# Kernel optimization log

Measured on AMD Instinct MI355X. Metric: run time of the kernel, lower is better.

The kernel has to match this reference:

```python
import jax, jax.numpy as jnp
import numpy as np
from jax import lax


def _ln(x, g, b, eps=1e-5):
    m = jnp.mean(x, axis=-1, keepdims=True)
    v = jnp.mean((x - m) ** 2, axis=-1, keepdims=True)
    return (x - m) / jnp.sqrt(v + eps) * g + b


def _lin(x, w, b):  # torch Linear: w [out,in]
    return x @ w.T + b


def _conv(x, w, b, stride, pad):
    y = lax.conv_general_dilated(x, w, (stride, stride), pad,
                                 dimension_numbers=('NCHW', 'OIHW', 'NCHW'))
    return y + b[None, :, None, None]


def _haar_dwt(x):
    # J=1 haar, zero mode, even H/W: per 2x2 block [[a,b],[c,d]]
    a = x[:, :, 0::2, 0::2]
    bb = x[:, :, 0::2, 1::2]
    c = x[:, :, 1::2, 0::2]
    d = x[:, :, 1::2, 1::2]
    ll = (a + bb + c + d) * 0.5
    lohi = (a - bb + c - d) * 0.5  # band 0 (col-high)
    hilo = (a + bb - c - d) * 0.5  # band 1 (row-high)
    hihi = (a - bb - c + d) * 0.5  # band 2
    return ll, lohi, hilo, hihi


def _cross_attention(q, k, v):
    # q,k,v: [b, d, c]; 8 equal chunks along d; softmax over QUERY axis (torch dim=1)
    b, d, c = q.shape
    chunk = d // 8
    qc = q.reshape(b, 8, chunk, c)
    kc = k.reshape(b, 8, chunk, c)
    vc = v.reshape(b, 8, chunk, c)
    att = jnp.einsum('bnqc,bnkc->bnqk', qc, kc) * (8.0 ** -0.5)
    att = jax.nn.softmax(att, axis=2)  # normalize over q (matches F.softmax dim=1)
    out = jnp.einsum('bnqk,bnkc->bnqc', att, vc)
    return out.reshape(b, d, c)


def _ffn(x, ln1_g, ln1_b, fc1_w, fc1_b, div_w, div_b, fc2_w, fc2_b,
         ln3_g, ln3_b, fc3a_w, fc3a_b, fc3b_w, fc3b_b, lnn_g, lnn_b, act_w, act_b):
    x1 = jax.nn.gelu(_lin(_ln(x, ln1_g, ln1_b), fc1_w, fc1_b), approximate=False)
    x2 = jax.nn.gelu(_lin(x, div_w, div_b), approximate=False) - x1
    x2 = jax.nn.gelu(_lin(x2, fc2_w, fc2_b), approximate=False)
    x3 = _lin(jax.nn.gelu(_lin(_ln(x, ln3_g, ln3_b), fc3a_w, fc3a_b), approximate=False), fc3b_w, fc3b_b)
    gate = jax.nn.sigmoid(_lin(x, act_w, act_b))
    # dropout(0.5) is identity in eval mode
    return gate * _ln(x2 + x3, lnn_g, lnn_b)


def _resize_bilinear_ac(x, oh, ow):
    # bilinear, align_corners=True
    B, C, H, W = x.shape
    def idx(n_in, n_out):
        pos = jnp.linspace(0.0, n_in - 1.0, n_out)
        i0 = jnp.floor(pos).astype(jnp.int32)
        i1 = jnp.minimum(i0 + 1, n_in - 1)
        return i0, i1, (pos - i0).astype(x.dtype)
    y0, y1, wy = idx(H, oh)
    x0, x1, wx = idx(W, ow)
    r = x[:, :, y0, :] * (1 - wy)[None, None, :, None] + x[:, :, y1, :] * wy[None, None, :, None]
    return r[:, :, :, x0] * (1 - wx)[None, None, None, :] + r[:, :, :, x1] * wx[None, None, None, :]


def setup_inputs() -> dict:
    key = jax.random.key(0)
    ks = jax.random.split(key, 25)
    B, Cin, H, W = 16, 128, 128, 128
    Ch = 128  # out_planes // 2
    def nrm(k, shp, s=0.02):
        return jax.random.normal(k, shp, jnp.float32) * s
    inp = {
        'x': jax.random.normal(ks[0], (B, Cin, H, W), jnp.float32),
        'conv1_w': nrm(ks[1], (Ch, 2 * Cin, 1, 1)), 'conv1_b': jnp.zeros((Ch,), jnp.float32),
        'l1_w': nrm(ks[2], (Ch, Cin, 4, 4)), 'l1_b': jnp.zeros((Ch,), jnp.float32),
        'ln1_g': jnp.ones((Ch,), jnp.float32), 'ln1_b': jnp.zeros((Ch,), jnp.float32),
        'fc1_w': nrm(ks[3], (Ch, Ch)), 'fc1_b': jnp.zeros((Ch,), jnp.float32),
        'div_w': nrm(ks[4], (Ch, Ch)), 'div_b': jnp.zeros((Ch,), jnp.float32),
        'fc2_w': nrm(ks[5], (Ch, Ch)), 'fc2_b': jnp.zeros((Ch,), jnp.float32),
        'ln3_g': jnp.ones((Ch,), jnp.float32), 'ln3_b': jnp.zeros((Ch,), jnp.float32),
        'fc3a_w': nrm(ks[6], (Ch, Ch)), 'fc3a_b': jnp.zeros((Ch,), jnp.float32),
        'fc3b_w': nrm(ks[7], (Ch, Ch)), 'fc3b_b': jnp.zeros((Ch,), jnp.float32),
        'lnn_g': jnp.ones((Ch,), jnp.float32), 'lnn_b': jnp.zeros((Ch,), jnp.float32),
        'act_w': nrm(ks[8], (Ch, Ch)), 'act_b': jnp.zeros((Ch,), jnp.float32),
    }
    return inp


def reference(x, conv1_w, conv1_b, l1_w, l1_b, ln1_g, ln1_b, fc1_w, fc1_b,
              div_w, div_b, fc2_w, fc2_b, ln3_g, ln3_b, fc3a_w, fc3a_b,
              fc3b_w, fc3b_b, lnn_g, lnn_b, act_w, act_b):
    dw = jax.nn.relu(_conv(x, l1_w, l1_b, 2, ((1, 1), (1, 1))))
    yL, y_HL, y_LH, y_HH = _haar_dwt(x)
    y = _conv(jnp.concatenate((y_HL, y_LH), axis=1), conv1_w, conv1_b, 1, ((0, 0), (0, 0)))
    b, c, h, w = y.shape
    y_t = y.transpose(0, 2, 3, 1).reshape(b, h * w, c)
    yL_t = yL.transpose(0, 2, 3, 1).reshape(b, h * w, c)
    yHH_t = y_HH.transpose(0, 2, 3, 1).reshape(b, h * w, c)
    att = _cross_attention(yL_t, y_t, yHH_t)
    att = _ffn(att, ln1_g, ln1_b, fc1_w, fc1_b, div_w, div_b, fc2_w, fc2_b,
               ln3_g, ln3_b, fc3a_w, fc3a_b, fc3b_w, fc3b_b, lnn_g, lnn_b, act_w, act_b)
    att = att.reshape(b, h, w, c).transpose(0, 3, 1, 2)
    y_img = y_t.reshape(b, h, w, c).transpose(0, 3, 1, 2)
    down_2x = _resize_bilinear_ac(x, h, w)
    att = att * (down_2x - dw)
    return att + y_img
```

## Files before the change

### kernel.cpp

```cpp
#include <hip/hip_runtime.h>
#include <cmath>


#define EPI_NONE 0
#define EPI_GELU 1
#define EPI_GELU_SUB 2
#define EPI_ADD 3
#define EPI_SIGMOID 4
#define EPI_EXP 5

typedef unsigned short u16;
typedef __bf16 v8bf __attribute__((ext_vector_type(8)));
typedef float f32x4 __attribute__((ext_vector_type(4)));

__device__ __forceinline__ float gelu_f(float v) {
  return 0.5f * v * (1.f + erff(v * 0.70710678118654752f));
}
__device__ __forceinline__ float sigmoid_f(float v) {
  return 1.f / (1.f + __expf(-v));
}
__device__ __forceinline__ float bf2f(u16 h) {
  return __uint_as_float((unsigned)h << 16);
}
__device__ __forceinline__ u16 f2bf(float f) {
  unsigned u = __float_as_uint(f);
  return (u16)((u + 0x7fffu + ((u >> 16) & 1u)) >> 16);
}
__device__ __forceinline__ unsigned f2bf_pk(float lo, float hi) {
  unsigned a = __float_as_uint(lo), b = __float_as_uint(hi);
  a = (a + 0x7fffu + ((a >> 16) & 1u)) >> 16;
  b = (b + 0x7fffu + ((b >> 16) & 1u)) >> 16;
  return a | (b << 16);
}

__global__ __launch_bounds__(256) void pre_k(const float* __restrict__ x,
                                             u16* __restrict__ yL16,
                                             u16* __restrict__ yHHt16,
                                             u16* __restrict__ hllh16) {
  int gx = blockIdx.x;
  int jt = gx & 1, cit = gx >> 1;
  int i = blockIdx.y, b = blockIdx.z;
  int j0 = jt * 32, ci0 = cit * 32;
  int tx = threadIdx.x & 31, ty = threadIdx.x >> 5;
  __shared__ float sll[32][33], shl[32][33], slh[32][33], shh[32][33];
  const float2* x2 = (const float2*)x;
#pragma unroll
  for (int k = 0; k < 4; ++k) {
    int ci = ty + 8 * k;
    long base = (((long)b * 128 + ci0 + ci) * 128 + 2 * i) * 64 + j0 + tx;
    float2 ab = x2[base];
    float2 cd = x2[base + 64];
    float a = ab.x, bb = ab.y, c = cd.x, d = cd.y;
    sll[ci][tx] = (a + bb + c + d) * 0.5f;
    shl[ci][tx] = (a - bb + c - d) * 0.5f;
    slh[ci][tx] = (a + bb - c - d) * 0.5f;
    shh[ci][tx] = (a - bb - c + d) * 0.5f;
  }
  __syncthreads();
  long tok = (long)b * 4096 + i * 64 + j0;
#pragma unroll
  for (int k = 0; k < 4; ++k) {
    int row = ty + 8 * k;
    long t = tok + row;
    yL16[t * 128 + ci0 + tx] = f2bf(sll[tx][row]);
    hllh16[t * 256 + ci0 + tx] = f2bf(shl[tx][row]);
    hllh16[t * 256 + 128 + ci0 + tx] = f2bf(slh[tx][row]);
    yHHt16[(long)(ci0 + row) * 65536 + tok + tx] = f2bf(shh[row][tx]);
  }
}

__global__ __launch_bounds__(256) void wcvt8_k(
    const float* __restrict__ a0, const float* __restrict__ a1,
    const float* __restrict__ a2, const float* __restrict__ a3,
    const float* __restrict__ a4, const float* __restrict__ a5,
    const float* __restrict__ a6, const float* __restrict__ a7,
    unsigned* __restrict__ dst) {
  int f = blockIdx.x * 256 + threadIdx.x;
  int e = 2 * f;
  const float* s; int b;
  if (e < 262144)      { s = a0; b = 0; }
  else if (e < 294912) { s = a1; b = 262144; }
  else if (e < 311296) { s = a2; b = 294912; }
  else if (e < 327680) { s = a3; b = 311296; }
  else if (e < 344064) { s = a4; b = 327680; }
  else if (e < 360448) { s = a5; b = 344064; }
  else if (e < 376832) { s = a6; b = 360448; }
  else                 { s = a7; b = 376832; }
  dst[f] = f2bf_pk(s[e - b], s[e - b + 1]);
}

template <int AMODE, int EPI>
__global__ __launch_bounds__(256) void gemm16_k(
    const u16* __restrict__ A, long sA, int lda,
    const u16* __restrict__ B, long sB, int ldb,
    u16* __restrict__ C, long sC, int ldc,
    int K, float alpha, const float* __restrict__ bias,
    const u16* __restrict__ aux, const float* __restrict__ sc) {
  __shared__ __align__(16) char smem[32768];
  char* As = smem;
  char* Bs = smem + 16384;
  int z = blockIdx.z;
  int tid = threadIdx.x, lane = tid & 63, w = tid >> 6;
  int wm = w >> 1, wn = w & 1, l15 = lane & 15, l4 = lane >> 4;
  const u16* Ab = A + (long)z * sA + (long)blockIdx.x * 128 * lda;
  const u16* Bb = B + (long)z * sB + (long)blockIdx.y * 128 * ldb;
  const float* scz = (AMODE == 1) ? sc + (long)z * K : nullptr;
  int sm = tid >> 3, skg = tid & 7;
  int sbase = sm * 128 + ((skg ^ (sm & 7)) << 4);
  uint4 pa[4], pb[4];

  auto loadAB = [&](int k0) {
#pragma unroll
    for (int u = 0; u < 4; ++u) {
      pb[u] = *(const uint4*)(Bb + (long)(sm + 32 * u) * ldb + k0 + skg * 8);
      uint4 v = *(const uint4*)(Ab + (long)(sm + 32 * u) * lda + k0 + skg * 8);
      if (AMODE == 1) {
        float4 s0 = *(const float4*)(scz + k0 + skg * 8);
        float4 s1 = *(const float4*)(scz + k0 + skg * 8 + 4);
        v.x = f2bf_pk(bf2f((u16)(v.x & 0xffff)) * s0.x, bf2f((u16)(v.x >> 16)) * s0.y);
        v.y = f2bf_pk(bf2f((u16)(v.y & 0xffff)) * s0.z, bf2f((u16)(v.y >> 16)) * s0.w);
        v.z = f2bf_pk(bf2f((u16)(v.z & 0xffff)) * s1.x, bf2f((u16)(v.z >> 16)) * s1.y);
        v.w = f2bf_pk(bf2f((u16)(v.w & 0xffff)) * s1.z, bf2f((u16)(v.w >> 16)) * s1.w);
      }
      pa[u] = v;
    }
  };

  f32x4 acc[4][4] = {};
  loadAB(0);
  int nch = K >> 6;
  for (int ch = 0; ch < nch; ++ch) {
    __syncthreads();
#pragma unroll
    for (int u = 0; u < 4; ++u) {
      *(uint4*)(As + sbase + u * 4096) = pa[u];
      *(uint4*)(Bs + sbase + u * 4096) = pb[u];
    }
    __syncthreads();
    if (ch + 1 < nch) loadAB((ch + 1) << 6);
#pragma unroll
    for (int s = 0; s < 2; ++s) {
      int ko = (((s << 2) | l4) ^ (l15 & 7)) << 4;
      v8bf af[4], bfr[4];
#pragma unroll
      for (int t = 0; t < 4; ++t) {
        af[t] = *(const v8bf*)(As + (64 * wm + 16 * t + l15) * 128 + ko);
        bfr[t] = *(const v8bf*)(Bs + (64 * wn + 16 * t + l15) * 128 + ko);
      }
#pragma unroll
      for (int mt = 0; mt < 4; ++mt)
#pragma unroll
        for (int nt = 0; nt < 4; ++nt)
          acc[mt][nt] = __builtin_amdgcn_mfma_f32_16x16x32_bf16(af[mt], bfr[nt], acc[mt][nt], 0, 0, 0);
    }
  }
  u16* Cb = C + (long)z * sC;
#pragma unroll
  for (int mt = 0; mt < 4; ++mt) {
#pragma unroll
    for (int nt = 0; nt < 4; ++nt) {
      f32x4 a = acc[mt][nt];
      int n = blockIdx.y * 128 + 64 * wn + 16 * nt + l15;
      float bv = bias ? bias[n] : 0.f;
#pragma unroll
      for (int r = 0; r < 4; ++r) {
        long m = (long)blockIdx.x * 128 + 64 * wm + 16 * mt + 4 * l4 + r;
        float v = a[r] * alpha + bv;
        if (EPI == EPI_GELU) v = gelu_f(v);
        else if (EPI == EPI_GELU_SUB) v = gelu_f(v) - bf2f(aux[m * ldc + n]);
        else if (EPI == EPI_ADD) v += bf2f(aux[m * ldc + n]);
        else if (EPI == EPI_SIGMOID) v = sigmoid_f(v);
        else if (EPI == EPI_EXP) v = __expf(v);
        Cb[m * ldc + n] = f2bf(v);
      }
    }
  }
}

__global__ __launch_bounds__(256) void conv4m_k(const float* __restrict__ x,
                                                const u16* __restrict__ wb,
                                                const float* __restrict__ bias,
                                                u16* __restrict__ dw16) {
  __shared__ __align__(16) char smem[36864];
  char* As = smem;
  char* Ws = smem + 18432;
  int ib = blockIdx.x, b = blockIdx.y;
  int tid = threadIdx.x;
  int lane = tid & 63, w = tid >> 6;
  int wm = w >> 1, wn = w & 1;
  int l15 = lane & 15, l4 = lane >> 4;
  f32x4 acc[4][4] = {};
  const float* xb = x + (long)b * 128 * 128 * 128;

  int m = tid & 127, qp0 = tid >> 7;
  int col0 = 2 * (m & 63) - 1;
  int oi_a = 2 * ib + (m >> 6);
  int groff = 2 * oi_a - 1;
  bool c0ok = (m & 63) != 0;
  bool c3ok = (m & 63) != 63;
  int awo[8];
#pragma unroll
  for (int it = 0; it < 8; ++it) awo[it] = m * 144 + (qp0 + 2 * it) * 8;
  const u16* wgbase = wb + (long)(tid >> 1) * 2048 + (tid & 1) * 32;
  int wro = (tid >> 1) * 144 + (tid & 1) * 64;

  uint4 wreg[4];
  uint2 areg[8];
  auto preW = [&](int ch) {
    const uint4* src = (const uint4*)(wgbase + ch * 64);
#pragma unroll
    for (int u = 0; u < 4; ++u) wreg[u] = src[u];
  };
  auto preA = [&](int ch) {
#pragma unroll
    for (int it = 0; it < 8; ++it) {
      int qp = qp0 + 2 * it;
      int c = qp >> 2, kh = qp & 3;
      int gr = groff + kh;
      const float* row = xb + ((long)(4 * ch + c) * 128 + gr) * 128;
      bool rok = (unsigned)gr < 128u;
      float v0 = (rok && c0ok) ? row[col0] : 0.f;
      float v1 = rok ? row[col0 + 1] : 0.f;
      float v2 = rok ? row[col0 + 2] : 0.f;
      float v3 = (rok && c3ok) ? row[col0 + 3] : 0.f;
      areg[it].x = f2bf_pk(v0, v1);
      areg[it].y = f2bf_pk(v2, v3);
    }
  };

  preW(0);
  preA(0);
  for (int ch = 0; ch < 32; ++ch) {
    __syncthreads();
    {
      uint4* dst = (uint4*)(Ws + wro);
#pragma unroll
      for (int u = 0; u < 4; ++u) dst[u] = wreg[u];
#pragma unroll
      for (int it = 0; it < 8; ++it) *(uint2*)(As + awo[it]) = areg[it];
    }
    __syncthreads();
    if (ch < 31) { preW(ch + 1); preA(ch + 1); }
#pragma unroll
    for (int s = 0; s < 2; ++s) {
      v8bf af[4], bfr[4];
#pragma unroll
      for (int t = 0; t < 4; ++t) {
        af[t] = *(const v8bf*)(As + (64 * wm + 16 * t + l15) * 144 + s * 64 + l4 * 16);
        bfr[t] = *(const v8bf*)(Ws + (64 * wn + 16 * t + l15) * 144 + s * 64 + l4 * 16);
      }
#pragma unroll
      for (int mt = 0; mt < 4; ++mt)
#pragma unroll
        for (int nt = 0; nt < 4; ++nt)
          acc[mt][nt] = __builtin_amdgcn_mfma_f32_16x16x32_bf16(af[mt], bfr[nt], acc[mt][nt], 0, 0, 0);
    }
  }
  __syncthreads();
  float* buf = (float*)(smem + w * 4352);
  int oi = 2 * ib + wm;
#pragma unroll
  for (int cg = 0; cg < 4; ++cg) {
    int co = 64 * wn + 16 * cg + l15;
    float bv = bias[co];
#pragma unroll
    for (int mt = 0; mt < 4; ++mt) {
      f32x4 a = acc[mt][cg];
#pragma unroll
      for (int r = 0; r < 4; ++r)
        buf[l15 * 65 + 16 * mt + 4 * l4 + r] = fmaxf(a[r] + bv, 0.f);
    }
    __syncthreads();
#pragma unroll
    for (int cr = 0; cr < 16; ++cr) {
      dw16[(((long)b * 128 + 64 * wn + 16 * cg + cr) * 64 + oi) * 64 + lane] =
          f2bf(buf[cr * 65 + lane]);
    }
    __syncthreads();
  }
}

__global__ __launch_bounds__(256) void ssum_k(const u16* __restrict__ E,
                                              float* __restrict__ sc) {
  int z = blockIdx.y;
  int k = blockIdx.x * 256 + threadIdx.x;
  const u16* Eb = E + (long)z * 262144 + k;
  float s = 0.f;
#pragma unroll 8
  for (int q = 0; q < 512; ++q) s += bf2f(Eb[(long)q * 512]);
  sc[(long)z * 512 + k] = 1.f / s;
}

__global__ __launch_bounds__(256) void ln16_k(const u16* __restrict__ X,
                                              const float* __restrict__ g,
                                              const float* __restrict__ bt,
                                              const u16* __restrict__ gate,
                                              u16* __restrict__ Y) {
  int t = (blockIdx.x * 256 + threadIdx.x) >> 6;
  int lane = threadIdx.x & 63;
  const u16* xr = X + (long)t * 128;
  float v0 = bf2f(xr[lane]), v1 = bf2f(xr[lane + 64]);
  float s = v0 + v1, sq = v0 * v0 + v1 * v1;
#pragma unroll
  for (int off = 32; off > 0; off >>= 1) {
    s += __shfl_xor(s, off);
    sq += __shfl_xor(sq, off);
  }
  float mean = s * 0.0078125f;
  float var = sq * 0.0078125f - mean * mean;
  float rstd = rsqrtf(var + 1e-5f);
  float y0 = (v0 - mean) * rstd * g[lane] + bt[lane];
  float y1 = (v1 - mean) * rstd * g[lane + 64] + bt[lane + 64];
  if (gate) {
    y0 *= bf2f(gate[(long)t * 128 + lane]);
    y1 *= bf2f(gate[(long)t * 128 + lane + 64]);
  }
  Y[(long)t * 128 + lane] = f2bf(y0);
  Y[(long)t * 128 + lane + 64] = f2bf(y1);
}

__global__ __launch_bounds__(256) void combine_k(const u16* __restrict__ attf,
                                                 const u16* __restrict__ yt,
                                                 const u16* __restrict__ dw16,
                                                 const float* __restrict__ x,
                                                 float* __restrict__ out) {
  int gx = blockIdx.x;
  int jt = gx & 1, cot = gx >> 1;
  int i = blockIdx.y, b = blockIdx.z;
  int j0 = jt * 32, co0 = cot * 32;
  int tx = threadIdx.x & 31, ty = threadIdx.x >> 5;
  __shared__ float sa[32][33], sy[32][33];
  long tokbase = (long)b * 4096 + i * 64 + j0;
#pragma unroll
  for (int k = 0; k < 4; ++k) {
    int row = ty + 8 * k;
    long idx = (tokbase + row) * 128 + co0 + tx;
    sa[row][tx] = bf2f(attf[idx]);
    sy[row][tx] = bf2f(yt[idx]);
  }
  __syncthreads();
  float py = (float)(i * 127) / 63.0f;
  int y0 = (int)py;
  int y1 = min(y0 + 1, 127);
  float wy = py - (float)y0;
  int j = j0 + tx;
  float px = (float)(j * 127) / 63.0f;
  int x0 = (int)px;
  int x1 = min(x0 + 1, 127);
  float wx = px - (float)x0;
#pragma unroll
  for (int k = 0; k < 4; ++k) {
    int co = co0 + ty + 8 * k;
    const float* xb = x + (((long)b * 128 + co) * 128) * 128;
    float r0 = xb[y0 * 128 + x0] * (1.f - wx) + xb[y0 * 128 + x1] * wx;
    float r1 = xb[y1 * 128 + x0] * (1.f - wx) + xb[y1 * 128 + x1] * wx;
    float d2 = r0 * (1.f - wy) + r1 * wy;
    long oidx = (((long)b * 128 + co) * 64 + i) * 64 + j;
    float dwv = bf2f(dw16[oidx]);
    out[oidx] = sa[tx][ty + 8 * k] * (d2 - dwv) + sy[tx][ty + 8 * k];
  }
}

extern "C" void kernel_launch(void* const* d_in, const int* in_sizes, int n_in,
                              void* d_out, int out_size, void* d_ws, size_t ws_size,
                              hipStream_t stream) {
  const float* x = (const float*)d_in[0];
  const float* w1 = (const float*)d_in[1];
  const float* b1 = (const float*)d_in[2];
  const float* l1w = (const float*)d_in[3];
  const float* l1b = (const float*)d_in[4];
  const float* ln1g = (const float*)d_in[5];
  const float* ln1b = (const float*)d_in[6];
  const float* fc1w = (const float*)d_in[7];
  const float* fc1b = (const float*)d_in[8];
  const float* divw = (const float*)d_in[9];
  const float* divb = (const float*)d_in[10];
  const float* fc2w = (const float*)d_in[11];
  const float* fc2b = (const float*)d_in[12];
  const float* ln3g = (const float*)d_in[13];
  const float* ln3b = (const float*)d_in[14];
  const float* fc3aw = (const float*)d_in[15];
  const float* fc3ab = (const float*)d_in[16];
  const float* fc3bw = (const float*)d_in[17];
  const float* fc3bb = (const float*)d_in[18];
  const float* lnng = (const float*)d_in[19];
  const float* lnnb = (const float*)d_in[20];
  const float* actw = (const float*)d_in[21];
  const float* actb = (const float*)d_in[22];

  char* W = (char*)d_ws;
  u16* yL16 = (u16*)(W);
  u16* hllh16 = (u16*)(W + 16777216L);
  u16* yHHt16 = (u16*)(W + 50331648L);
  u16* y16 = (u16*)(W + 67108864L);
  u16* S16 = (u16*)(W + 83886080L);
  u16* attO16 = (u16*)(W + 150994944L);
  u16* dw16 = (u16*)(W + 167772160L);
  u16* t1 = (u16*)(W + 184549376L);
  u16* t2 = (u16*)(W + 201326592L);
  u16* t3 = (u16*)(W + 218103808L);
  u16* t4 = (u16*)(W + 234881024L);
  float* sc = (float*)(W + 251658240L);
  u16* wall = (u16*)(W + 251920384L);
  u16* l1wb = wall;
  u16* w1b = wall + 262144;
  u16* fc1b16 = wall + 294912;
  u16* divb16 = wall + 311296;
  u16* fc2b16 = wall + 327680;
  u16* fc3ab16 = wall + 344064;
  u16* fc3bb16 = wall + 360448;
  u16* actb16 = wall + 376832;

  dim3 blk(256);
  const float qk_scale = 0.35355339059327373f;

  wcvt8_k<<<dim3(768), blk, 0, stream>>>(l1w, w1, fc1w, divw, fc2w, fc3aw,
                                         fc3bw, actw, (unsigned*)wall);
  pre_k<<<dim3(8, 64, 16), blk, 0, stream>>>(x, yL16, yHHt16, hllh16);
  gemm16_k<0, EPI_NONE><<<dim3(512, 1, 1), blk, 0, stream>>>(
      hllh16, 0, 256, w1b, 0, 256, y16, 0, 128, 256, 1.f, b1, nullptr, nullptr);
  conv4m_k<<<dim3(32, 16), blk, 0, stream>>>(x, l1wb, l1b, dw16);
  gemm16_k<0, EPI_EXP><<<dim3(4, 4, 128), blk, 0, stream>>>(
      yL16, 65536, 128, y16, 65536, 128, S16, 262144, 512, 128, qk_scale,
      nullptr, nullptr, nullptr);
  ssum_k<<<dim3(2, 128), blk, 0, stream>>>(S16, sc);
  gemm16_k<1, EPI_NONE><<<dim3(4, 1, 128), blk, 0, stream>>>(
      S16, 262144, 512, yHHt16, 512, 65536, attO16, 65536, 128, 512, 1.f,
      nullptr, nullptr, sc);
  ln16_k<<<16384, blk, 0, stream>>>(attO16, ln1g, ln1b, nullptr, t1);
  gemm16_k<0, EPI_GELU><<<dim3(512, 1, 1), blk, 0, stream>>>(
      t1, 0, 128, fc1b16, 0, 128, t2, 0, 128, 128, 1.f, fc1b, nullptr, nullptr);
  gemm16_k<0, EPI_GELU_SUB><<<dim3(512, 1, 1), blk, 0, stream>>>(
      attO16, 0, 128, divb16, 0, 128, t3, 0, 128, 128, 1.f, divb, t2, nullptr);
  gemm16_k<0, EPI_GELU><<<dim3(512, 1, 1), blk, 0, stream>>>(
      t3, 0, 128, fc2b16, 0, 128, t4, 0, 128, 128, 1.f, fc2b, nullptr, nullptr);
  ln16_k<<<16384, blk, 0, stream>>>(attO16, ln3g, ln3b, nullptr, t1);
  gemm16_k<0, EPI_GELU><<<dim3(512, 1, 1), blk, 0, stream>>>(
      t1, 0, 128, fc3ab16, 0, 128, t3, 0, 128, 128, 1.f, fc3ab, nullptr, nullptr);
  gemm16_k<0, EPI_ADD><<<dim3(512, 1, 1), blk, 0, stream>>>(
      t3, 0, 128, fc3bb16, 0, 128, t1, 0, 128, 128, 1.f, fc3bb, t4, nullptr);
  gemm16_k<0, EPI_SIGMOID><<<dim3(512, 1, 1), blk, 0, stream>>>(
      attO16, 0, 128, actb16, 0, 128, t3, 0, 128, 128, 1.f, actb, nullptr, nullptr);
  ln16_k<<<16384, blk, 0, stream>>>(t1, lnng, lnnb, t3, t2);
  combine_k<<<dim3(8, 64, 16), blk, 0, stream>>>(t2, y16, dw16, x, (float*)d_out);
}
```

Measured before the change: 754.9 us.

## Rewrite stride-2 conv using bf16 polyphase input produced by the DWT prepass

```diff
diff --git a/kernel.cpp b/kernel.cpp
--- a/kernel.cpp
+++ b/kernel.cpp
@@ -36,7 +36,8 @@
 __global__ __launch_bounds__(256) void pre_k(const float* __restrict__ x,
                                              u16* __restrict__ yL16,
                                              u16* __restrict__ yHHt16,
-                                             u16* __restrict__ hllh16) {
+                                             u16* __restrict__ hllh16,
+                                             u16* __restrict__ xpt) {
   int gx = blockIdx.x;
   int jt = gx & 1, cit = gx >> 1;
   int i = blockIdx.y, b = blockIdx.z;
@@ -58,14 +59,26 @@
   }
   __syncthreads();
   long tok = (long)b * 4096 + i * 64 + j0;
+  const long PLS = 64L * 64 * 128;
 #pragma unroll
   for (int k = 0; k < 4; ++k) {
     int row = ty + 8 * k;
     long t = tok + row;
-    yL16[t * 128 + ci0 + tx] = f2bf(sll[tx][row]);
-    hllh16[t * 256 + ci0 + tx] = f2bf(shl[tx][row]);
-    hllh16[t * 256 + 128 + ci0 + tx] = f2bf(slh[tx][row]);
+    float ll = sll[tx][row], hl = shl[tx][row], lh = slh[tx][row],
+          hh = shh[tx][row];
+    yL16[t * 128 + ci0 + tx] = f2bf(ll);
+    hllh16[t * 256 + ci0 + tx] = f2bf(hl);
+    hllh16[t * 256 + 128 + ci0 + tx] = f2bf(lh);
     yHHt16[(long)(ci0 + row) * 65536 + tok + tx] = f2bf(shh[row][tx]);
+    float pa = 0.5f * (ll + hl + lh + hh);
+    float pb = 0.5f * (ll - hl + lh - hh);
+    float pc = 0.5f * (ll + hl - lh - hh);
+    float pd = 0.5f * (ll - hl - lh + hh);
+    long pbase = (((long)b * 4 * 64 + i) * 64 + (j0 + row)) * 128 + ci0 + tx;
+    xpt[pbase] = f2bf(pa);
+    xpt[pbase + PLS] = f2bf(pb);
+    xpt[pbase + 2 * PLS] = f2bf(pc);
+    xpt[pbase + 3 * PLS] = f2bf(pd);
   }
 }
 
@@ -77,9 +90,20 @@
     unsigned* __restrict__ dst) {
   int f = blockIdx.x * 256 + threadIdx.x;
   int e = 2 * f;
+  if (e < 262144) {
+    int n = e >> 11, k = e & 2047;
+    int chunk = k >> 6, klocal = k & 63;
+    int stg = chunk >> 2, sub = chunk & 3;
+    int kwsel = sub >> 1, chalf = sub & 1;
+    int kh = stg >> 1, cp = stg & 1;
+    int kw = cp ? (kwsel ? 2 : 0) : (kwsel ? 3 : 1);
+    int c = chalf * 64 + klocal;
+    long si = (((long)n * 128 + c) * 4 + kh) * 4 + kw;
+    dst[f] = f2bf_pk(a0[si], a0[si + 16]);
+    return;
+  }
   const float* s; int b;
-  if (e < 262144)      { s = a0; b = 0; }
-  else if (e < 294912) { s = a1; b = 262144; }
+  if (e < 294912)      { s = a1; b = 262144; }
   else if (e < 311296) { s = a2; b = 294912; }
   else if (e < 327680) { s = a3; b = 311296; }
   else if (e < 344064) { s = a4; b = 327680; }
@@ -177,104 +201,125 @@
   }
 }
 
-__global__ __launch_bounds__(256) void conv4m_k(const float* __restrict__ x,
-                                                const u16* __restrict__ wb,
-                                                const float* __restrict__ bias,
-                                                u16* __restrict__ dw16) {
-  __shared__ __align__(16) char smem[36864];
+__global__ __launch_bounds__(256, 4) void conv4p_k(
+    const u16* __restrict__ xpt, const u16* __restrict__ wb,
+    const float* __restrict__ bias, u16* __restrict__ dw16) {
+  __shared__ __align__(16) char smem[33024];
   char* As = smem;
-  char* Ws = smem + 18432;
-  int ib = blockIdx.x, b = blockIdx.y;
-  int tid = threadIdx.x;
-  int lane = tid & 63, w = tid >> 6;
-  int wm = w >> 1, wn = w & 1;
-  int l15 = lane & 15, l4 = lane >> 4;
-  f32x4 acc[4][4] = {};
-  const float* xb = x + (long)b * 128 * 128 * 128;
-
-  int m = tid & 127, qp0 = tid >> 7;
-  int col0 = 2 * (m & 63) - 1;
-  int oi_a = 2 * ib + (m >> 6);
-  int groff = 2 * oi_a - 1;
-  bool c0ok = (m & 63) != 0;
-  bool c3ok = (m & 63) != 63;
-  int awo[8];
-#pragma unroll
-  for (int it = 0; it < 8; ++it) awo[it] = m * 144 + (qp0 + 2 * it) * 8;
-  const u16* wgbase = wb + (long)(tid >> 1) * 2048 + (tid & 1) * 32;
-  int wro = (tid >> 1) * 144 + (tid & 1) * 64;
-
-  uint4 wreg[4];
-  uint2 areg[8];
-  auto preW = [&](int ch) {
-    const uint4* src = (const uint4*)(wgbase + ch * 64);
-#pragma unroll
-    for (int u = 0; u < 4; ++u) wreg[u] = src[u];
+  char* Ws = smem + 16640;
+  int raw = blockIdx.x;
+  int swz = (raw & 7) * 128 + (raw >> 3);
+  int oi = swz & 63, b = swz >> 6;
+  int tid = threadIdx.x, lane = tid & 63, w = tid >> 6;
+  int wm = w >> 1, wn = w & 1, l15 = lane & 15, l4 = lane >> 4;
+  f32x4 acc[2][4] = {};
+  const long PLS = 64L * 64 * 128;
+  const u16* xb = xpt + (long)b * 4 * PLS;
+
+  uint4 aReg[5], wReg[4];
+
+  auto preW = [&](int chunk) {
+#pragma unroll
+    for (int r = 0; r < 4; ++r) {
+      int u = r * 256 + tid;
+      int row = u >> 3, kg = u & 7;
+      wReg[r] = *(const uint4*)(wb + (long)row * 2048 + chunk * 64 + kg * 8);
+    }
   };
-  auto preA = [&](int ch) {
-#pragma unroll
-    for (int it = 0; it < 8; ++it) {
-      int qp = qp0 + 2 * it;
-      int c = qp >> 2, kh = qp & 3;
-      int gr = groff + kh;
-      const float* row = xb + ((long)(4 * ch + c) * 128 + gr) * 128;
-      bool rok = (unsigned)gr < 128u;
-      float v0 = (rok && c0ok) ? row[col0] : 0.f;
-      float v1 = rok ? row[col0 + 1] : 0.f;
-      float v2 = rok ? row[col0 + 2] : 0.f;
-      float v3 = (rok && c3ok) ? row[col0 + 3] : 0.f;
-      areg[it].x = f2bf_pk(v0, v1);
-      areg[it].y = f2bf_pk(v2, v3);
+  auto preA = [&](int stg) {
+    int kh = stg >> 1, cp = stg & 1;
+    int roff = (kh == 0) ? -1 : (kh == 3) ? 1 : 0;
+    int ri = oi + roff;
+    int ph = (((kh + 1) & 1) << 1) | cp;
+    const u16* pp = xb + (long)ph * PLS + (long)ri * 8192;
+    bool rok = (unsigned)ri < 64u;
+#pragma unroll
+    for (int r = 0; r < 5; ++r) {
+      int u = r * 256 + tid;
+      int slot = u >> 4, cg = u & 15;
+      int ci = slot - cp;
+      bool ok = rok && (unsigned)ci < 64u && (r < 4 || tid < 16);
+      aReg[r] = ok ? *(const uint4*)(pp + (long)ci * 128 + cg * 8)
+                   : uint4{0u, 0u, 0u, 0u};
     }
   };
-
+  auto writeA = [&]() {
+#pragma unroll
+    for (int r = 0; r < 5; ++r) {
+      if (r < 4 || tid < 16) {
+        int u = r * 256 + tid;
+        int slot = u >> 4, cg = u & 15;
+        *(uint4*)(As + slot * 256 + ((cg ^ (slot & 7)) << 4)) = aReg[r];
+      }
+    }
+  };
+  auto writeW = [&]() {
+#pragma unroll
+    for (int r = 0; r < 4; ++r) {
+      int u = r * 256 + tid;
+      int row = u >> 3, kg = u & 7;
+      *(uint4*)(Ws + row * 128 + ((kg ^ (row & 7)) << 4)) = wReg[r];
+    }
+  };
+
+  preA(0);
   preW(0);
-  preA(0);
-  for (int ch = 0; ch < 32; ++ch) {
-    __syncthreads();
-    {
-      uint4* dst = (uint4*)(Ws + wro);
-#pragma unroll
-      for (int u = 0; u < 4; ++u) dst[u] = wreg[u];
-#pragma unroll
-      for (int it = 0; it < 8; ++it) *(uint2*)(As + awo[it]) = areg[it];
-    }
-    __syncthreads();
-    if (ch < 31) { preW(ch + 1); preA(ch + 1); }
-#pragma unroll
-    for (int s = 0; s < 2; ++s) {
-      v8bf af[4], bfr[4];
-#pragma unroll
-      for (int t = 0; t < 4; ++t) {
-        af[t] = *(const v8bf*)(As + (64 * wm + 16 * t + l15) * 144 + s * 64 + l4 * 16);
-        bfr[t] = *(const v8bf*)(Ws + (64 * wn + 16 * t + l15) * 144 + s * 64 + l4 * 16);
+  for (int stg = 0; stg < 8; ++stg) {
+#pragma unroll
+    for (int sub = 0; sub < 4; ++sub) {
+      __syncthreads();
+      if (sub == 0) writeA();
+      writeW();
+      __syncthreads();
+      int chunk = stg * 4 + sub;
+      if (chunk < 31) preW(chunk + 1);
+      if (sub == 0 && stg < 7) preA(stg + 1);
+      const int kwsel = sub >> 1, chalf = sub & 1;
+#pragma unroll
+      for (int s = 0; s < 2; ++s) {
+        v8bf af[2], bw[4];
+#pragma unroll
+        for (int mt = 0; mt < 2; ++mt) {
+          int slot = 32 * wm + 16 * mt + l15 + kwsel;
+          int cg = chalf * 8 + s * 4 + l4;
+          af[mt] = *(const v8bf*)(As + slot * 256 + ((cg ^ (slot & 7)) << 4));
+        }
+#pragma unroll
+        for (int nt = 0; nt < 4; ++nt) {
+          int row = 64 * wn + 16 * nt + l15;
+          int kg = s * 4 + l4;
+          bw[nt] = *(const v8bf*)(Ws + row * 128 + ((kg ^ (row & 7)) << 4));
+        }
+#pragma unroll
+        for (int mt = 0; mt < 2; ++mt)
+#pragma unroll
+          for (int nt = 0; nt < 4; ++nt)
+            acc[mt][nt] = __builtin_amdgcn_mfma_f32_16x16x32_bf16(
+                af[mt], bw[nt], acc[mt][nt], 0, 0, 0);
       }
-#pragma unroll
-      for (int mt = 0; mt < 4; ++mt)
-#pragma unroll
-        for (int nt = 0; nt < 4; ++nt)
-          acc[mt][nt] = __builtin_amdgcn_mfma_f32_16x16x32_bf16(af[mt], bfr[nt], acc[mt][nt], 0, 0, 0);
     }
   }
   __syncthreads();
-  float* buf = (float*)(smem + w * 4352);
-  int oi = 2 * ib + wm;
+  float* buf = (float*)(smem + w * 2176);
+  long obase = ((long)b * 128) * 4096 + oi * 64;
 #pragma unroll
   for (int cg = 0; cg < 4; ++cg) {
     int co = 64 * wn + 16 * cg + l15;
     float bv = bias[co];
 #pragma unroll
-    for (int mt = 0; mt < 4; ++mt) {
+    for (int mt = 0; mt < 2; ++mt) {
       f32x4 a = acc[mt][cg];
 #pragma unroll
       for (int r = 0; r < 4; ++r)
-        buf[l15 * 65 + 16 * mt + 4 * l4 + r] = fmaxf(a[r] + bv, 0.f);
+        buf[l15 * 34 + 16 * mt + 4 * l4 + r] = fmaxf(a[r] + bv, 0.f);
     }
     __syncthreads();
 #pragma unroll
-    for (int cr = 0; cr < 16; ++cr) {
-      dw16[(((long)b * 128 + 64 * wn + 16 * cg + cr) * 64 + oi) * 64 + lane] =
-          f2bf(buf[cr * 65 + lane]);
+    for (int it = 0; it < 8; ++it) {
+      int row = it * 2 + (lane >> 5);
+      int mcol = lane & 31;
+      int coz = 64 * wn + 16 * cg + row;
+      dw16[obase + (long)coz * 4096 + 32 * wm + mcol] = f2bf(buf[row * 34 + mcol]);
     }
     __syncthreads();
   }
@@ -410,16 +455,17 @@
   u16* fc3ab16 = wall + 344064;
   u16* fc3bb16 = wall + 360448;
   u16* actb16 = wall + 376832;
+  u16* xpt16 = S16;
 
   dim3 blk(256);
   const float qk_scale = 0.35355339059327373f;
 
   wcvt8_k<<<dim3(768), blk, 0, stream>>>(l1w, w1, fc1w, divw, fc2w, fc3aw,
                                          fc3bw, actw, (unsigned*)wall);
-  pre_k<<<dim3(8, 64, 16), blk, 0, stream>>>(x, yL16, yHHt16, hllh16);
+  pre_k<<<dim3(8, 64, 16), blk, 0, stream>>>(x, yL16, yHHt16, hllh16, xpt16);
   gemm16_k<0, EPI_NONE><<<dim3(512, 1, 1), blk, 0, stream>>>(
       hllh16, 0, 256, w1b, 0, 256, y16, 0, 128, 256, 1.f, b1, nullptr, nullptr);
-  conv4m_k<<<dim3(32, 16), blk, 0, stream>>>(x, l1wb, l1b, dw16);
+  conv4p_k<<<dim3(1024), blk, 0, stream>>>(xpt16, l1wb, l1b, dw16);
   gemm16_k<0, EPI_EXP><<<dim3(4, 4, 128), blk, 0, stream>>>(
       yL16, 65536, 128, y16, 65536, 128, S16, 262144, 512, 128, qk_scale,
       nullptr, nullptr, nullptr);
```

Result: slower. 800.0 us (+6.0%).
